# Optimization experiments

Measured on AMD Instinct MI355X. Metric: run time of the kernel, lower is better.

Reference implementation:

```python
import jax, jax.numpy as jnp
import numpy as np

THR = 10.0           # spike threshold (all layers, igarss2023 config)
LEAK1, LEAK2, LEAK3 = 9.0, 1.0, 0.0  # subtractive leak per layer
POOL1_K, POOL1_S = 7, 6
POOL2_K, POOL2_S = 2, 2
WTA_BLOCK = 2        # local spatial WTA window


def conv2d_same(x, w):
    # x: (B,C,H,W), w: (O,I,kh,kw)
    return jax.lax.conv_general_dilated(
        x, w, window_strides=(1, 1), padding='SAME',
        dimension_numbers=('NCHW', 'OIHW', 'NCHW'))


def maxpool(x, k, s):
    return jax.lax.reduce_window(
        x, -jnp.inf, jax.lax.max, (1, 1, k, k), (1, 1, s, s), 'VALID')


def wta(mem, spk, block=WTA_BLOCK):
    """Winner-take-all lateral inhibition ('both' mode):
    (1) channel competition: only the channel with max membrane at each
        spatial location may spike; (2) local spatial competition: only the
        max-membrane neuron within each block x block window of each map
        may spike. Requires H,W divisible by block."""
    C = mem.shape[1]
    ch_win = jnp.argmax(mem, axis=1)                         # (B,H,W)
    ch_mask = jax.nn.one_hot(ch_win, C, axis=1, dtype=mem.dtype)  # (B,C,H,W)
    loc = jax.lax.reduce_window(
        mem, -jnp.inf, jax.lax.max,
        (1, 1, block, block), (1, 1, block, block), 'VALID')
    loc_up = jnp.repeat(jnp.repeat(loc, block, axis=2), block, axis=3)
    sp_mask = (mem >= loc_up).astype(mem.dtype)
    return spk * ch_mask * sp_mask


def lif_step(mem, inp, leak, use_wta):
    # integrate -> threshold -> WTA -> reset-to-zero -> subtractive leak
    mem = mem + inp
    spk = (mem >= THR).astype(mem.dtype)
    if use_wta:
        spk = wta(mem, spk)
    mem = jnp.where(spk > 0, 0.0, mem)
    mem = jnp.maximum(mem - leak, 0.0)
    return mem, spk


def setup_inputs() -> dict:
    key = jax.random.key(0)
    k0, k1, k2, k3 = jax.random.split(key, 4)
    T, B, H, W = 20, 8, 256, 256
    x = jax.random.uniform(k0, (T, B, 1, H, W), dtype=jnp.float32)
    # STDP-style weights are non-negative in [0,1)
    w1 = jax.random.uniform(k1, (4, 1, 5, 5), dtype=jnp.float32)
    w2 = jax.random.uniform(k2, (36, 4, 5, 5), dtype=jnp.float32)
    w3 = jax.random.uniform(k3, (1, 36, 7, 7), dtype=jnp.float32)
    return {"x": x, "w1": w1, "w2": w2, "w3": w3}


def reference(x, w1, w2, w3):
    T, B, _, H, W = x.shape
    H1, W1 = H, W                                   # conv1 SAME
    H2 = (H1 - POOL1_K) // POOL1_S + 1              # 42
    W2 = (W1 - POOL1_K) // POOL1_S + 1
    H3 = (H2 - POOL2_K) // POOL2_S + 1              # 21
    W3 = (W2 - POOL2_K) // POOL2_S + 1
    C1, C2, C3 = w1.shape[0], w2.shape[0], w3.shape[0]

    m1_0 = jnp.zeros((B, C1, H1, W1), x.dtype)
    m2_0 = jnp.zeros((B, C2, H2, W2), x.dtype)
    m3_0 = jnp.zeros((B, C3, H3, W3), x.dtype)

    def step(carry, xt):
        m1, m2, m3 = carry
        m1, s1 = lif_step(m1, conv2d_same(xt, w1), LEAK1, True)
        p1 = maxpool(s1, POOL1_K, POOL1_S)
        m2, s2 = lif_step(m2, conv2d_same(p1, w2), LEAK2, True)
        p2 = maxpool(s2, POOL2_K, POOL2_S)
        m3, s3 = lif_step(m3, conv2d_same(p2, w3), LEAK3, False)
        return (m1, m2, m3), s3

    _, cls_spikes = jax.lax.scan(step, (m1_0, m2_0, m3_0), x)
    return cls_spikes  # (T, B, n_classes, H3, W3)
```

## Files before the change

### kernel.cpp

```cpp
#include <hip/hip_runtime.h>
#include <stdint.h>

#define THR 10.0f
#define AGT __HIP_MEMORY_SCOPE_AGENT

static constexpr size_t OFF_P2  = 1048576;
static constexpr size_t OFF_BAR = 1245184;

static __device__ __forceinline__ uint32_t ldu32(const uint32_t* p) {
    return __hip_atomic_load(p, __ATOMIC_RELAXED, AGT);
}
static __device__ __forceinline__ void stu32(uint32_t* p, uint32_t v) {
    __hip_atomic_store(p, v, __ATOMIC_RELAXED, AGT);
}
static __device__ __forceinline__ void stu16(uint16_t* p, uint16_t v) {
    __hip_atomic_store(p, v, __ATOMIC_RELAXED, AGT);
}
static __device__ __forceinline__ uint32_t rmwread(uint32_t* p) {
    return __hip_atomic_fetch_add(p, 0u, __ATOMIC_RELAXED, AGT);
}

__global__ __launch_bounds__(256) void zero_bar(uint32_t* __restrict__ bar) {
    if (threadIdx.x < 256) bar[threadIdx.x] = 0u;
}

__device__ __forceinline__ void gbar(uint32_t* bar, int bid, uint32_t n) {
    __syncthreads();
    if (threadIdx.x == 0) {
        uint32_t* base = bar + (bid >> 6) * 32;
        uint32_t a = __hip_atomic_fetch_add(base, 1u, __ATOMIC_RELAXED, AGT);
        if (a == 64u * n - 1u)
            __hip_atomic_fetch_add(base + 16, 1u, __ATOMIC_RELAXED, AGT);
        while (rmwread(base + 16) < n)
            __builtin_amdgcn_s_sleep(2);
    }
    __syncthreads();
}

__global__ __launch_bounds__(256, 2) void spike_persist(
    const float* __restrict__ x,
    const float* __restrict__ w1,
    const float* __restrict__ w2,
    const float* __restrict__ w3,
    float* __restrict__ out,
    uint8_t* __restrict__ s1b,
    uint8_t* __restrict__ p2b,
    uint32_t* __restrict__ bar)
{
    __shared__ union {
        float    xs[2112];
        uint32_t st32[527];
    } u;
    __shared__ float    ps[400];
    __shared__ float    mem_s[1296];
    __shared__ float    bm_s[324];
    __shared__ int      wc_s[36];
    __shared__ uint32_t p2a[18];

    const int tid = threadIdx.x;
    const int bid = blockIdx.x;
    uint32_t nbar = 0;

    const int b1 = bid >> 6;
    const int r0 = (bid & 63) * 4;
    const int tr = tid >> 7, tc = tid & 127;
    const int py = r0 + 2 * tr;
    const int px = 2 * tc;

    const int tIdx = bid & 63;
    const int b2 = bid >> 6;
    const int tyi = tIdx >> 3, txi = tIdx & 7;
    const int oy2 = tyi < 5 ? 6 * tyi : 30 + 4 * (tyi - 5);
    const int ox2 = txi < 5 ? 6 * txi : 30 + 4 * (txi - 5);
    const int th2 = tyi < 5 ? 6 : 4;
    const int tw2 = txi < 5 ? 6 : 4;
    const int wave = tid >> 6, lane = tid & 63;
    const int pr = lane / 6, pc = lane - 6 * pr;
    const bool act = (pr < th2) && (pc < tw2);
    const int prA = pr > 5 ? 0 : pr, pcA = pc;

    const int lid3 = (bid & 63) * 4 + wave;
    const int kyl = lane / 7, kxl = lane % 7;

    float w3v[36];
#pragma unroll
    for (int c = 0; c < 36; c++) w3v[c] = (lane < 49) ? w3[c * 49 + lane] : 0.f;

    float m1r[4][2][2];
#pragma unroll
    for (int c = 0; c < 4; c++)
#pragma unroll
        for (int dy = 0; dy < 2; dy++)
#pragma unroll
            for (int dx = 0; dx < 2; dx++) m1r[c][dy][dx] = 0.f;
    float m2r[9];
#pragma unroll
    for (int i = 0; i < 9; i++) m2r[i] = 0.f;
    float m3r[2] = {0.f, 0.f};

    for (int k = 0; k < 12; k++) {
        for (int tt = 0; tt < 2; tt++) {
            const int t = 2 * k + tt;
            if (t >= 20) break;
            uint16_t* s1w = reinterpret_cast<uint16_t*>(s1b + (size_t)(t & 3) * 262144);
            const float* xb = x + ((size_t)t * 8 + b1) * 65536;
            __syncthreads();
#pragma unroll
            for (int i = 0; i < 9; i++) {
                int idx = tid + i * 256;
                if (idx < 2112) {
                    int row = idx / 264, col = idx - row * 264;
                    int gy = r0 + row - 2, gx = col - 2;
                    float v = 0.f;
                    if (gy >= 0 && gy < 256 && gx >= 0 && gx < 256) v = xb[gy * 256 + gx];
                    u.xs[idx] = v;
                }
            }
            __syncthreads();

            float p[6][6];
#pragma unroll
            for (int i = 0; i < 6; i++)
#pragma unroll
                for (int j = 0; j < 6; j++)
                    p[i][j] = u.xs[(2 * tr + i) * 264 + 2 * tc + j];

            float acc[4][2][2];
#pragma unroll
            for (int c = 0; c < 4; c++)
#pragma unroll
                for (int dy = 0; dy < 2; dy++)
#pragma unroll
                    for (int dx = 0; dx < 2; dx++) acc[c][dy][dx] = 0.f;
#pragma unroll
            for (int c = 0; c < 4; c++)
#pragma unroll
                for (int ky = 0; ky < 5; ky++)
#pragma unroll
                    for (int kx = 0; kx < 5; kx++) {
                        float w = w1[c * 25 + ky * 5 + kx];
#pragma unroll
                        for (int dy = 0; dy < 2; dy++)
#pragma unroll
                            for (int dx = 0; dx < 2; dx++)
                                acc[c][dy][dx] = fmaf(p[dy + ky][dx + kx], w, acc[c][dy][dx]);
                    }

            float mem[4][2][2];
#pragma unroll
            for (int c = 0; c < 4; c++)
#pragma unroll
                for (int dy = 0; dy < 2; dy++)
#pragma unroll
                    for (int dx = 0; dx < 2; dx++)
                        mem[c][dy][dx] = m1r[c][dy][dx] + acc[c][dy][dx];

            int wc[2][2];
#pragma unroll
            for (int dy = 0; dy < 2; dy++)
#pragma unroll
                for (int dx = 0; dx < 2; dx++) {
                    int w = 0; float mx = mem[0][dy][dx];
#pragma unroll
                    for (int c = 1; c < 4; c++) {
                        float v = mem[c][dy][dx];
                        if (v > mx) { mx = v; w = c; }
                    }
                    wc[dy][dx] = w;
                }

            float bm[4];
#pragma unroll
            for (int c = 0; c < 4; c++)
                bm[c] = fmaxf(fmaxf(mem[c][0][0], mem[c][0][1]), fmaxf(mem[c][1][0], mem[c][1][1]));

            uint32_t bits = 0;
#pragma unroll
            for (int c = 0; c < 4; c++)
#pragma unroll
                for (int dy = 0; dy < 2; dy++)
#pragma unroll
                    for (int dx = 0; dx < 2; dx++) {
                        float m = mem[c][dy][dx];
                        bool s = (m >= THR) && (wc[dy][dx] == c) && (m >= bm[c]);
                        m1r[c][dy][dx] = fmaxf((s ? 0.f : m) - 9.0f, 0.f);
                        bits |= (s ? 1u : 0u) << (c * 4 + dy * 2 + dx);
                    }
            stu16(s1w + ((size_t)(b1 * 128 + (r0 >> 1) + tr)) * 128 + tc, (uint16_t)bits);
        }

        for (int tt = 0; tt < 2; tt++) {
            const int tl = 2 * k - 4 + tt;
            if (tl < 0 || tl >= 20) continue;
            const uint32_t* pb32 = reinterpret_cast<const uint32_t*>(
                p2b + (size_t)(tl % 6) * 32768);
#pragma unroll
            for (int rep = 0; rep < 2; rep++) {
                int o = lid3 + rep * 256;
                if (o < 441) {
                    int rr = o / 21, cl = o - rr * 21;
                    int yy = rr + kyl - 3, xx = cl + kxl - 3;
                    bool inb = (lane < 49) && yy >= 0 && yy < 21 && xx >= 0 && xx < 21;
                    uint32_t lo = 0, hi = 0;
                    if (inb) {
                        const uint32_t* pc = pb32 + (((size_t)b2 * 441 + yy * 21 + xx) << 1);
                        lo = ldu32(pc);
                        hi = ldu32(pc + 1);
                    }
                    float accv = 0.f;
#pragma unroll
                    for (int c = 0; c < 32; c++) accv += ((lo >> c) & 1u) ? w3v[c] : 0.f;
#pragma unroll
                    for (int c = 0; c < 4; c++)  accv += ((hi >> c) & 1u) ? w3v[32 + c] : 0.f;
#pragma unroll
                    for (int off = 32; off; off >>= 1) accv += __shfl_xor(accv, off, 64);
                    float memv3 = m3r[rep] + accv;
                    bool s = memv3 >= THR;
                    if (lane == 0) out[(size_t)tl * 3528 + b2 * 441 + o] = s ? 1.f : 0.f;
                    m3r[rep] = fmaxf(s ? 0.f : memv3, 0.f);
                }
            }
        }

        for (int tt = 0; tt < 2; tt++) {
            const int tb = 2 * k - 2 + tt;
            if (tb < 0 || tb >= 20) continue;
            const uint32_t* s1r32 = reinterpret_cast<const uint32_t*>(
                s1b + (size_t)(tb & 3) * 262144);
            uint32_t* p2w32 = reinterpret_cast<uint32_t*>(p2b + (size_t)(tb % 6) * 32768);

            const int rb0 = 3 * oy2 - 6;
            const int cb0 = (3 * ox2 - 6) >> 1;

            __syncthreads();
#pragma unroll
            for (int i = 0; i < 3; i++) {
                int idx = tid + i * 256;
                if (idx < 527) {
                    int row = idx / 17, w = idx - row * 17;
                    int grow = rb0 + row, gcol = cb0 + w;
                    uint32_t v = 0;
                    if (grow >= 0 && grow < 128 && gcol >= 0 && gcol < 64)
                        v = ldu32(s1r32 + ((size_t)b2 * 128 + grow) * 64 + gcol);
                    u.st32[idx] = v;
                }
            }
            __syncthreads();

            if (tid < 100) {
                int r = tid / 10, cc2 = tid - 10 * r;
                int gy = oy2 - 2 + r, gx = ox2 - 2 + cc2;
                uint32_t accb = 0;
                if (r < th2 + 4 && cc2 < tw2 + 4 && gy >= 0 && gy < 42 && gx >= 0 && gx < 42) {
                    const uint16_t* st16 = reinterpret_cast<const uint16_t*>(u.st32);
#pragma unroll
                    for (int kr = 0; kr < 4; kr++)
#pragma unroll
                        for (int kc = 0; kc < 4; kc++) {
                            uint32_t m = (kr < 3) ? (kc < 3 ? 0xFu : 0x5u)
                                                  : (kc < 3 ? 0x3u : 0x1u);
                            uint32_t v = st16[(3 * r + kr) * 34 + 3 * cc2 + kc];
                            accb |= v & (m * 0x1111u);
                        }
                }
#pragma unroll
                for (int ic = 0; ic < 4; ic++)
                    ps[ic * 100 + tid] = ((accb >> (4 * ic)) & 0xFu) ? 1.f : 0.f;
            }
            __syncthreads();

            float pv[4][5][5];
#pragma unroll
            for (int ic = 0; ic < 4; ic++)
#pragma unroll
                for (int i = 0; i < 5; i++)
#pragma unroll
                    for (int j = 0; j < 5; j++)
                        pv[ic][i][j] = ps[ic * 100 + (prA + i) * 10 + (pcA + j)];

            float memv[9];
            for (int cc = 0; cc < 9; cc++) {
                int c = cc * 4 + wave;
                const float* wr = w2 + (size_t)__builtin_amdgcn_readfirstlane(c) * 100;
                float accv = 0.f;
#pragma unroll
                for (int ic = 0; ic < 4; ic++)
#pragma unroll
                    for (int i = 0; i < 5; i++)
#pragma unroll
                        for (int j = 0; j < 5; j++)
                            accv = fmaf(pv[ic][i][j], wr[ic * 25 + i * 5 + j], accv);
                float m = act ? (m2r[cc] + accv) : -1e30f;
                memv[cc] = m;
                if (lane < 36) mem_s[c * 36 + lane] = m;
            }
            __syncthreads();

            if (tid < 36) {
                float mx = mem_s[tid]; int w = 0;
#pragma unroll
                for (int c = 1; c < 36; c++) {
                    float v = mem_s[c * 36 + tid];
                    if (v > mx) { mx = v; w = c; }
                }
                wc_s[tid] = w;
            }
#pragma unroll
            for (int i = 0; i < 2; i++) {
                int idx = tid + i * 256;
                if (idx < 324) {
                    int c = idx / 9, blk = idx - 9 * c;
                    int br = blk / 3, bc2 = blk - 3 * br;
                    int l0 = 12 * br + 2 * bc2;
                    float a = mem_s[c * 36 + l0],     bb2 = mem_s[c * 36 + l0 + 1];
                    float d = mem_s[c * 36 + l0 + 6], e   = mem_s[c * 36 + l0 + 7];
                    bm_s[idx] = fmaxf(fmaxf(a, bb2), fmaxf(d, e));
                }
            }
            if (tid < 18) p2a[tid] = 0;
            __syncthreads();

            const int blkl = (pr >> 1) * 3 + (pc >> 1);
            for (int cc = 0; cc < 9; cc++) {
                int c = cc * 4 + wave;
                if (act) {
                    float m = memv[cc];
                    bool s = (m >= THR) && (wc_s[lane] == c) && (m >= bm_s[c * 9 + blkl]);
                    m2r[cc] = fmaxf((s ? 0.f : m) - 1.0f, 0.f);
                }
            }

#pragma unroll
            for (int i = 0; i < 2; i++) {
                int idx = tid + i * 256;
                if (idx < 324) {
                    int c = idx / 9, blk = idx - 9 * c;
                    int br = blk / 3, bc2 = blk - 3 * br;
                    if (2 * br < th2 && 2 * bc2 < tw2) {
                        int l0 = 12 * br + 2 * bc2;
                        float bmv = bm_s[idx];
                        bool any = false;
#pragma unroll
                        for (int kk = 0; kk < 4; kk++) {
                            int l = l0 + (kk >> 1) * 6 + (kk & 1);
                            float m = mem_s[c * 36 + l];
                            any |= (m >= THR) && (wc_s[l] == c) && (m >= bmv);
                        }
                        if (any)
                            atomicOr(&p2a[(blk << 1) + (c >> 5)], 1u << (c & 31));
                    }
                }
            }
            __syncthreads();

            if (tid < 9) {
                int br = tid / 3, bc2 = tid - 3 * br;
                if (2 * br < th2 && 2 * bc2 < tw2) {
                    int cell = b2 * 441 + ((oy2 >> 1) + br) * 21 + (ox2 >> 1) + bc2;
                    uint32_t* dst = p2w32 + ((size_t)cell << 1);
                    stu32(dst, p2a[tid * 2]);
                    stu32(dst + 1, p2a[tid * 2 + 1]);
                }
            }
        }

        if (k < 11) gbar(bar, bid, ++nbar);
    }
}

extern "C" void kernel_launch(void* const* d_in, const int* in_sizes, int n_in,
                              void* d_out, int out_size, void* d_ws, size_t ws_size,
                              hipStream_t stream) {
    const float* x  = (const float*)d_in[0];
    const float* w1 = (const float*)d_in[1];
    const float* w2 = (const float*)d_in[2];
    const float* w3 = (const float*)d_in[3];
    float* out = (float*)d_out;
    uint8_t* s1 = (uint8_t*)d_ws;
    uint8_t* p2 = (uint8_t*)d_ws + OFF_P2;
    uint32_t* bar = (uint32_t*)((char*)d_ws + OFF_BAR);

    zero_bar<<<1, 256, 0, stream>>>(bar);

    void* args[] = {(void*)&x, (void*)&w1, (void*)&w2, (void*)&w3,
                    (void*)&out, (void*)&s1, (void*)&p2, (void*)&bar};
    hipLaunchCooperativeKernel((void*)spike_persist, dim3(512), dim3(256),
                               args, 0, stream);
}
```

Before: 459.1 us.

## Batch four timesteps per grid barrier and prefetch cross-stage inputs into registers

Each pipeline stage now processes four timesteps between grid barriers instead of two, cutting the number of grid-wide barriers from 11 to 6. The stage-1 and pooled-spike ring buffers grow from 4/6 slots to 8, and the workspace offsets are enlarged to fit. Stage-2 and stage-3 inputs for all four timesteps are loaded into registers at the start of each round, and the address and bounds math is hoisted out of the loop. The cost is deeper pipeline fill and drain, higher register pressure from the prefetch arrays, and a larger workspace.

```diff
diff --git a/kernel.cpp b/kernel.cpp
--- a/kernel.cpp
+++ b/kernel.cpp
@@ -4,8 +4,8 @@
 #define THR 10.0f
 #define AGT __HIP_MEMORY_SCOPE_AGENT
 
-static constexpr size_t OFF_P2  = 1048576;
-static constexpr size_t OFF_BAR = 1245184;
+static constexpr size_t OFF_P2  = 2097152;
+static constexpr size_t OFF_BAR = 2359296;
 
 static __device__ __forceinline__ uint32_t ldu32(const uint32_t* p) {
     return __hip_atomic_load(p, __ATOMIC_RELAXED, AGT);
@@ -64,8 +64,6 @@
     const int b1 = bid >> 6;
     const int r0 = (bid & 63) * 4;
     const int tr = tid >> 7, tc = tid & 127;
-    const int py = r0 + 2 * tr;
-    const int px = 2 * tc;
 
     const int tIdx = bid & 63;
     const int b2 = bid >> 6;
@@ -86,6 +84,40 @@
 #pragma unroll
     for (int c = 0; c < 36; c++) w3v[c] = (lane < 49) ? w3[c * 49 + lane] : 0.f;
 
+    int aoff[9]; bool aval[9];
+#pragma unroll
+    for (int i = 0; i < 9; i++) {
+        int idx = tid + i * 256;
+        int row = idx / 264, col = idx - row * 264;
+        int gy = r0 + row - 2, gx = col - 2;
+        aval[i] = (idx < 2112) && gy >= 0 && gy < 256 && gx >= 0 && gx < 256;
+        aoff[i] = gy * 256 + gx;
+    }
+    const size_t s1soff = ((size_t)(b1 * 128 + (r0 >> 1) + tr)) * 128 + tc;
+
+    const int rb0 = 3 * oy2 - 6;
+    const int cb0 = (3 * ox2 - 6) >> 1;
+    int boff[3]; bool bval[3];
+#pragma unroll
+    for (int i = 0; i < 3; i++) {
+        int idx = tid + i * 256;
+        int row = idx / 17, w = idx - row * 17;
+        int grow = rb0 + row, gcol = cb0 + w;
+        bval[i] = (idx < 527) && grow >= 0 && grow < 128 && gcol >= 0 && gcol < 64;
+        boff[i] = (b2 * 128 + grow) * 64 + gcol;
+    }
+
+    bool l3in[2], l3v[2]; int l3o[2];
+#pragma unroll
+    for (int rep = 0; rep < 2; rep++) {
+        int o = lid3 + rep * 256;
+        int rr = o / 21, cl = o - rr * 21;
+        int yy = rr + kyl - 3, xx = cl + kxl - 3;
+        l3in[rep] = o < 441;
+        l3v[rep] = (o < 441) && (lane < 49) && yy >= 0 && yy < 21 && xx >= 0 && xx < 21;
+        l3o[rep] = (b2 * 441 + yy * 21 + xx) << 1;
+    }
+
     float m1r[4][2][2];
 #pragma unroll
     for (int c = 0; c < 4; c++)
@@ -98,273 +130,282 @@
     for (int i = 0; i < 9; i++) m2r[i] = 0.f;
     float m3r[2] = {0.f, 0.f};
 
-    for (int k = 0; k < 12; k++) {
-        for (int tt = 0; tt < 2; tt++) {
-            const int t = 2 * k + tt;
-            if (t >= 20) break;
-            uint16_t* s1w = reinterpret_cast<uint16_t*>(s1b + (size_t)(t & 3) * 262144);
-            const float* xb = x + ((size_t)t * 8 + b1) * 65536;
-            __syncthreads();
-#pragma unroll
-            for (int i = 0; i < 9; i++) {
-                int idx = tid + i * 256;
-                if (idx < 2112) {
-                    int row = idx / 264, col = idx - row * 264;
-                    int gy = r0 + row - 2, gx = col - 2;
-                    float v = 0.f;
-                    if (gy >= 0 && gy < 256 && gx >= 0 && gx < 256) v = xb[gy * 256 + gx];
-                    u.xs[idx] = v;
-                }
-            }
-            __syncthreads();
-
-            float p[6][6];
-#pragma unroll
-            for (int i = 0; i < 6; i++)
-#pragma unroll
-                for (int j = 0; j < 6; j++)
-                    p[i][j] = u.xs[(2 * tr + i) * 264 + 2 * tc + j];
-
-            float acc[4][2][2];
-#pragma unroll
-            for (int c = 0; c < 4; c++)
-#pragma unroll
-                for (int dy = 0; dy < 2; dy++)
-#pragma unroll
-                    for (int dx = 0; dx < 2; dx++) acc[c][dy][dx] = 0.f;
-#pragma unroll
-            for (int c = 0; c < 4; c++)
-#pragma unroll
-                for (int ky = 0; ky < 5; ky++)
-#pragma unroll
-                    for (int kx = 0; kx < 5; kx++) {
-                        float w = w1[c * 25 + ky * 5 + kx];
-#pragma unroll
-                        for (int dy = 0; dy < 2; dy++)
-#pragma unroll
-                            for (int dx = 0; dx < 2; dx++)
-                                acc[c][dy][dx] = fmaf(p[dy + ky][dx + kx], w, acc[c][dy][dx]);
-                    }
-
-            float mem[4][2][2];
-#pragma unroll
-            for (int c = 0; c < 4; c++)
-#pragma unroll
-                for (int dy = 0; dy < 2; dy++)
-#pragma unroll
-                    for (int dx = 0; dx < 2; dx++)
-                        mem[c][dy][dx] = m1r[c][dy][dx] + acc[c][dy][dx];
-
-            int wc[2][2];
-#pragma unroll
-            for (int dy = 0; dy < 2; dy++)
-#pragma unroll
-                for (int dx = 0; dx < 2; dx++) {
-                    int w = 0; float mx = mem[0][dy][dx];
-#pragma unroll
-                    for (int c = 1; c < 4; c++) {
-                        float v = mem[c][dy][dx];
-                        if (v > mx) { mx = v; w = c; }
-                    }
-                    wc[dy][dx] = w;
-                }
-
-            float bm[4];
-#pragma unroll
-            for (int c = 0; c < 4; c++)
-                bm[c] = fmaxf(fmaxf(mem[c][0][0], mem[c][0][1]), fmaxf(mem[c][1][0], mem[c][1][1]));
-
-            uint32_t bits = 0;
-#pragma unroll
-            for (int c = 0; c < 4; c++)
-#pragma unroll
-                for (int dy = 0; dy < 2; dy++)
-#pragma unroll
-                    for (int dx = 0; dx < 2; dx++) {
-                        float m = mem[c][dy][dx];
-                        bool s = (m >= THR) && (wc[dy][dx] == c) && (m >= bm[c]);
-                        m1r[c][dy][dx] = fmaxf((s ? 0.f : m) - 9.0f, 0.f);
-                        bits |= (s ? 1u : 0u) << (c * 4 + dy * 2 + dx);
-                    }
-            stu16(s1w + ((size_t)(b1 * 128 + (r0 >> 1) + tr)) * 128 + tc, (uint16_t)bits);
-        }
-
-        for (int tt = 0; tt < 2; tt++) {
-            const int tl = 2 * k - 4 + tt;
-            if (tl < 0 || tl >= 20) continue;
-            const uint32_t* pb32 = reinterpret_cast<const uint32_t*>(
-                p2b + (size_t)(tl % 6) * 32768);
-#pragma unroll
-            for (int rep = 0; rep < 2; rep++) {
-                int o = lid3 + rep * 256;
-                if (o < 441) {
-                    int rr = o / 21, cl = o - rr * 21;
-                    int yy = rr + kyl - 3, xx = cl + kxl - 3;
-                    bool inb = (lane < 49) && yy >= 0 && yy < 21 && xx >= 0 && xx < 21;
-                    uint32_t lo = 0, hi = 0;
-                    if (inb) {
-                        const uint32_t* pc = pb32 + (((size_t)b2 * 441 + yy * 21 + xx) << 1);
-                        lo = ldu32(pc);
-                        hi = ldu32(pc + 1);
-                    }
-                    float accv = 0.f;
-#pragma unroll
-                    for (int c = 0; c < 32; c++) accv += ((lo >> c) & 1u) ? w3v[c] : 0.f;
-#pragma unroll
-                    for (int c = 0; c < 4; c++)  accv += ((hi >> c) & 1u) ? w3v[32 + c] : 0.f;
-#pragma unroll
-                    for (int off = 32; off; off >>= 1) accv += __shfl_xor(accv, off, 64);
-                    float memv3 = m3r[rep] + accv;
-                    bool s = memv3 >= THR;
-                    if (lane == 0) out[(size_t)tl * 3528 + b2 * 441 + o] = s ? 1.f : 0.f;
-                    m3r[rep] = fmaxf(s ? 0.f : memv3, 0.f);
-                }
+    for (int k = 0; k < 7; k++) {
+        uint32_t pfB[4][3];
+#pragma unroll
+        for (int tt = 0; tt < 4; tt++) {
+            int tb = 4 * k - 4 + tt;
+            if (tb >= 0 && tb < 20) {
+                const uint32_t* s1r32 = reinterpret_cast<const uint32_t*>(
+                    s1b + (size_t)(tb & 7) * 262144);
+#pragma unroll
+                for (int i = 0; i < 3; i++)
+                    pfB[tt][i] = bval[i] ? ldu32(s1r32 + boff[i]) : 0u;
             }
         }
-
-        for (int tt = 0; tt < 2; tt++) {
-            const int tb = 2 * k - 2 + tt;
-            if (tb < 0 || tb >= 20) continue;
-            const uint32_t* s1r32 = reinterpret_cast<const uint32_t*>(
-                s1b + (size_t)(tb & 3) * 262144);
-            uint32_t* p2w32 = reinterpret_cast<uint32_t*>(p2b + (size_t)(tb % 6) * 32768);
-
-            const int rb0 = 3 * oy2 - 6;
-            const int cb0 = (3 * ox2 - 6) >> 1;
-
-            __syncthreads();
-#pragma unroll
-            for (int i = 0; i < 3; i++) {
-                int idx = tid + i * 256;
-                if (idx < 527) {
-                    int row = idx / 17, w = idx - row * 17;
-                    int grow = rb0 + row, gcol = cb0 + w;
-                    uint32_t v = 0;
-                    if (grow >= 0 && grow < 128 && gcol >= 0 && gcol < 64)
-                        v = ldu32(s1r32 + ((size_t)b2 * 128 + grow) * 64 + gcol);
-                    u.st32[idx] = v;
-                }
-            }
-            __syncthreads();
-
-            if (tid < 100) {
-                int r = tid / 10, cc2 = tid - 10 * r;
-                int gy = oy2 - 2 + r, gx = ox2 - 2 + cc2;
-                uint32_t accb = 0;
-                if (r < th2 + 4 && cc2 < tw2 + 4 && gy >= 0 && gy < 42 && gx >= 0 && gx < 42) {
-                    const uint16_t* st16 = reinterpret_cast<const uint16_t*>(u.st32);
-#pragma unroll
-                    for (int kr = 0; kr < 4; kr++)
-#pragma unroll
-                        for (int kc = 0; kc < 4; kc++) {
-                            uint32_t m = (kr < 3) ? (kc < 3 ? 0xFu : 0x5u)
-                                                  : (kc < 3 ? 0x3u : 0x1u);
-                            uint32_t v = st16[(3 * r + kr) * 34 + 3 * cc2 + kc];
-                            accb |= v & (m * 0x1111u);
-                        }
-                }
-#pragma unroll
-                for (int ic = 0; ic < 4; ic++)
-                    ps[ic * 100 + tid] = ((accb >> (4 * ic)) & 0xFu) ? 1.f : 0.f;
-            }
-            __syncthreads();
-
-            float pv[4][5][5];
-#pragma unroll
-            for (int ic = 0; ic < 4; ic++)
-#pragma unroll
-                for (int i = 0; i < 5; i++)
-#pragma unroll
-                    for (int j = 0; j < 5; j++)
-                        pv[ic][i][j] = ps[ic * 100 + (prA + i) * 10 + (pcA + j)];
-
-            float memv[9];
-            for (int cc = 0; cc < 9; cc++) {
-                int c = cc * 4 + wave;
-                const float* wr = w2 + (size_t)__builtin_amdgcn_readfirstlane(c) * 100;
-                float accv = 0.f;
-#pragma unroll
-                for (int ic = 0; ic < 4; ic++)
-#pragma unroll
-                    for (int i = 0; i < 5; i++)
-#pragma unroll
-                        for (int j = 0; j < 5; j++)
-                            accv = fmaf(pv[ic][i][j], wr[ic * 25 + i * 5 + j], accv);
-                float m = act ? (m2r[cc] + accv) : -1e30f;
-                memv[cc] = m;
-                if (lane < 36) mem_s[c * 36 + lane] = m;
-            }
-            __syncthreads();
-
-            if (tid < 36) {
-                float mx = mem_s[tid]; int w = 0;
-#pragma unroll
-                for (int c = 1; c < 36; c++) {
-                    float v = mem_s[c * 36 + tid];
-                    if (v > mx) { mx = v; w = c; }
-                }
-                wc_s[tid] = w;
-            }
-#pragma unroll
-            for (int i = 0; i < 2; i++) {
-                int idx = tid + i * 256;
-                if (idx < 324) {
-                    int c = idx / 9, blk = idx - 9 * c;
-                    int br = blk / 3, bc2 = blk - 3 * br;
-                    int l0 = 12 * br + 2 * bc2;
-                    float a = mem_s[c * 36 + l0],     bb2 = mem_s[c * 36 + l0 + 1];
-                    float d = mem_s[c * 36 + l0 + 6], e   = mem_s[c * 36 + l0 + 7];
-                    bm_s[idx] = fmaxf(fmaxf(a, bb2), fmaxf(d, e));
-                }
-            }
-            if (tid < 18) p2a[tid] = 0;
-            __syncthreads();
-
-            const int blkl = (pr >> 1) * 3 + (pc >> 1);
-            for (int cc = 0; cc < 9; cc++) {
-                int c = cc * 4 + wave;
-                if (act) {
-                    float m = memv[cc];
-                    bool s = (m >= THR) && (wc_s[lane] == c) && (m >= bm_s[c * 9 + blkl]);
-                    m2r[cc] = fmaxf((s ? 0.f : m) - 1.0f, 0.f);
-                }
-            }
-
-#pragma unroll
-            for (int i = 0; i < 2; i++) {
-                int idx = tid + i * 256;
-                if (idx < 324) {
-                    int c = idx / 9, blk = idx - 9 * c;
-                    int br = blk / 3, bc2 = blk - 3 * br;
-                    if (2 * br < th2 && 2 * bc2 < tw2) {
-                        int l0 = 12 * br + 2 * bc2;
-                        float bmv = bm_s[idx];
-                        bool any = false;
-#pragma unroll
-                        for (int kk = 0; kk < 4; kk++) {
-                            int l = l0 + (kk >> 1) * 6 + (kk & 1);
-                            float m = mem_s[c * 36 + l];
-                            any |= (m >= THR) && (wc_s[l] == c) && (m >= bmv);
-                        }
-                        if (any)
-                            atomicOr(&p2a[(blk << 1) + (c >> 5)], 1u << (c & 31));
-                    }
-                }
-            }
-            __syncthreads();
-
-            if (tid < 9) {
-                int br = tid / 3, bc2 = tid - 3 * br;
-                if (2 * br < th2 && 2 * bc2 < tw2) {
-                    int cell = b2 * 441 + ((oy2 >> 1) + br) * 21 + (ox2 >> 1) + bc2;
-                    uint32_t* dst = p2w32 + ((size_t)cell << 1);
-                    stu32(dst, p2a[tid * 2]);
-                    stu32(dst + 1, p2a[tid * 2 + 1]);
+        uint32_t pfLlo[4][2], pfLhi[4][2];
+#pragma unroll
+        for (int tt = 0; tt < 4; tt++) {
+            int tl = 4 * k - 8 + tt;
+            if (tl >= 0 && tl < 20) {
+                const uint32_t* pb32 = reinterpret_cast<const uint32_t*>(
+                    p2b + (size_t)(tl & 7) * 32768);
+#pragma unroll
+                for (int rep = 0; rep < 2; rep++) {
+                    pfLlo[tt][rep] = l3v[rep] ? ldu32(pb32 + l3o[rep]) : 0u;
+                    pfLhi[tt][rep] = l3v[rep] ? ldu32(pb32 + l3o[rep] + 1) : 0u;
                 }
             }
         }
 
-        if (k < 11) gbar(bar, bid, ++nbar);
+#pragma unroll
+        for (int tt = 0; tt < 4; tt++) {
+            const int t = 4 * k + tt;
+            if (t < 20) {
+                uint16_t* s1w = reinterpret_cast<uint16_t*>(s1b + (size_t)(t & 7) * 262144);
+                const float* xb = x + ((size_t)t * 8 + b1) * 65536;
+                __syncthreads();
+#pragma unroll
+                for (int i = 0; i < 9; i++) {
+                    int idx = tid + i * 256;
+                    if (idx < 2112) u.xs[idx] = aval[i] ? xb[aoff[i]] : 0.f;
+                }
+                __syncthreads();
+
+                const float2* xs2 = reinterpret_cast<const float2*>(u.xs);
+                float p[6][6];
+#pragma unroll
+                for (int i = 0; i < 6; i++)
+#pragma unroll
+                    for (int j = 0; j < 3; j++) {
+                        float2 v = xs2[(2 * tr + i) * 132 + tc + j];
+                        p[i][2 * j] = v.x; p[i][2 * j + 1] = v.y;
+                    }
+
+                float acc[4][2][2];
+#pragma unroll
+                for (int c = 0; c < 4; c++)
+#pragma unroll
+                    for (int dy = 0; dy < 2; dy++)
+#pragma unroll
+                        for (int dx = 0; dx < 2; dx++) acc[c][dy][dx] = 0.f;
+#pragma unroll
+                for (int c = 0; c < 4; c++)
+#pragma unroll
+                    for (int ky = 0; ky < 5; ky++)
+#pragma unroll
+                        for (int kx = 0; kx < 5; kx++) {
+                            float w = w1[c * 25 + ky * 5 + kx];
+#pragma unroll
+                            for (int dy = 0; dy < 2; dy++)
+#pragma unroll
+                                for (int dx = 0; dx < 2; dx++)
+                                    acc[c][dy][dx] = fmaf(p[dy + ky][dx + kx], w, acc[c][dy][dx]);
+                        }
+
+                float mem[4][2][2];
+#pragma unroll
+                for (int c = 0; c < 4; c++)
+#pragma unroll
+                    for (int dy = 0; dy < 2; dy++)
+#pragma unroll
+                        for (int dx = 0; dx < 2; dx++)
+                            mem[c][dy][dx] = m1r[c][dy][dx] + acc[c][dy][dx];
+
+                int wc[2][2];
+#pragma unroll
+                for (int dy = 0; dy < 2; dy++)
+#pragma unroll
+                    for (int dx = 0; dx < 2; dx++) {
+                        int w = 0; float mx = mem[0][dy][dx];
+#pragma unroll
+                        for (int c = 1; c < 4; c++) {
+                            float v = mem[c][dy][dx];
+                            if (v > mx) { mx = v; w = c; }
+                        }
+                        wc[dy][dx] = w;
+                    }
+
+                float bm[4];
+#pragma unroll
+                for (int c = 0; c < 4; c++)
+                    bm[c] = fmaxf(fmaxf(mem[c][0][0], mem[c][0][1]),
+                                  fmaxf(mem[c][1][0], mem[c][1][1]));
+
+                uint32_t bits = 0;
+#pragma unroll
+                for (int c = 0; c < 4; c++)
+#pragma unroll
+                    for (int dy = 0; dy < 2; dy++)
+#pragma unroll
+                        for (int dx = 0; dx < 2; dx++) {
+                            float m = mem[c][dy][dx];
+                            bool s = (m >= THR) && (wc[dy][dx] == c) && (m >= bm[c]);
+                            m1r[c][dy][dx] = fmaxf((s ? 0.f : m) - 9.0f, 0.f);
+                            bits |= (s ? 1u : 0u) << (c * 4 + dy * 2 + dx);
+                        }
+                stu16(reinterpret_cast<uint16_t*>(s1w) + s1soff, (uint16_t)bits);
+            }
+        }
+
+#pragma unroll
+        for (int tt = 0; tt < 4; tt++) {
+            const int tl = 4 * k - 8 + tt;
+            if (tl >= 0 && tl < 20) {
+#pragma unroll
+                for (int rep = 0; rep < 2; rep++) {
+                    if (l3in[rep]) {
+                        int o = lid3 + rep * 256;
+                        uint32_t lo = pfLlo[tt][rep], hi = pfLhi[tt][rep];
+                        float accv = 0.f;
+#pragma unroll
+                        for (int c = 0; c < 32; c++) accv += ((lo >> c) & 1u) ? w3v[c] : 0.f;
+#pragma unroll
+                        for (int c = 0; c < 4; c++)  accv += ((hi >> c) & 1u) ? w3v[32 + c] : 0.f;
+#pragma unroll
+                        for (int off = 32; off; off >>= 1) accv += __shfl_xor(accv, off, 64);
+                        float memv3 = m3r[rep] + accv;
+                        bool s = memv3 >= THR;
+                        if (lane == 0) out[(size_t)tl * 3528 + b2 * 441 + o] = s ? 1.f : 0.f;
+                        m3r[rep] = fmaxf(s ? 0.f : memv3, 0.f);
+                    }
+                }
+            }
+        }
+
+#pragma unroll
+        for (int tt = 0; tt < 4; tt++) {
+            const int tb = 4 * k - 4 + tt;
+            if (tb >= 0 && tb < 20) {
+                uint32_t* p2w32 = reinterpret_cast<uint32_t*>(p2b + (size_t)(tb & 7) * 32768);
+
+                __syncthreads();
+#pragma unroll
+                for (int i = 0; i < 3; i++) {
+                    int idx = tid + i * 256;
+                    if (idx < 527) u.st32[idx] = pfB[tt][i];
+                }
+                __syncthreads();
+
+                if (tid < 100) {
+                    int r = tid / 10, cc2 = tid - 10 * r;
+                    int gy = oy2 - 2 + r, gx = ox2 - 2 + cc2;
+                    uint32_t accb = 0;
+                    if (r < th2 + 4 && cc2 < tw2 + 4 && gy >= 0 && gy < 42 && gx >= 0 && gx < 42) {
+                        const uint16_t* st16 = reinterpret_cast<const uint16_t*>(u.st32);
+#pragma unroll
+                        for (int kr = 0; kr < 4; kr++)
+#pragma unroll
+                            for (int kc = 0; kc < 4; kc++) {
+                                uint32_t m = (kr < 3) ? (kc < 3 ? 0xFu : 0x5u)
+                                                      : (kc < 3 ? 0x3u : 0x1u);
+                                uint32_t v = st16[(3 * r + kr) * 34 + 3 * cc2 + kc];
+                                accb |= v & (m * 0x1111u);
+                            }
+                    }
+#pragma unroll
+                    for (int ic = 0; ic < 4; ic++)
+                        ps[ic * 100 + tid] = ((accb >> (4 * ic)) & 0xFu) ? 1.f : 0.f;
+                }
+                __syncthreads();
+
+                float pv[4][5][5];
+#pragma unroll
+                for (int ic = 0; ic < 4; ic++)
+#pragma unroll
+                    for (int i = 0; i < 5; i++)
+#pragma unroll
+                        for (int j = 0; j < 5; j++)
+                            pv[ic][i][j] = ps[ic * 100 + (prA + i) * 10 + (pcA + j)];
+
+                float memv[9];
+                for (int cc = 0; cc < 9; cc++) {
+                    int c = cc * 4 + wave;
+                    const float* wr = w2 + (size_t)__builtin_amdgcn_readfirstlane(c) * 100;
+                    float accv = 0.f;
+#pragma unroll
+                    for (int ic = 0; ic < 4; ic++)
+#pragma unroll
+                        for (int i = 0; i < 5; i++)
+#pragma unroll
+                            for (int j = 0; j < 5; j++)
+                                accv = fmaf(pv[ic][i][j], wr[ic * 25 + i * 5 + j], accv);
+                    float m = act ? (m2r[cc] + accv) : -1e30f;
+                    memv[cc] = m;
+                    if (lane < 36) mem_s[c * 36 + lane] = m;
+                }
+                __syncthreads();
+
+                if (tid < 36) {
+                    float mx = mem_s[tid]; int w = 0;
+#pragma unroll
+                    for (int c = 1; c < 36; c++) {
+                        float v = mem_s[c * 36 + tid];
+                        if (v > mx) { mx = v; w = c; }
+                    }
+                    wc_s[tid] = w;
+                }
+#pragma unroll
+                for (int i = 0; i < 2; i++) {
+                    int idx = tid + i * 256;
+                    if (idx < 324) {
+                        int c = idx / 9, blk = idx - 9 * c;
+                        int br = blk / 3, bc2 = blk - 3 * br;
+                        int l0 = 12 * br + 2 * bc2;
+                        float a = mem_s[c * 36 + l0],     bb2 = mem_s[c * 36 + l0 + 1];
+                        float d = mem_s[c * 36 + l0 + 6], e   = mem_s[c * 36 + l0 + 7];
+                        bm_s[idx] = fmaxf(fmaxf(a, bb2), fmaxf(d, e));
+                    }
+                }
+                if (tid < 18) p2a[tid] = 0;
+                __syncthreads();
+
+                const int blkl = (pr >> 1) * 3 + (pc >> 1);
+                for (int cc = 0; cc < 9; cc++) {
+                    int c = cc * 4 + wave;
+                    if (act) {
+                        float m = memv[cc];
+                        bool s = (m >= THR) && (wc_s[lane] == c) && (m >= bm_s[c * 9 + blkl]);
+                        m2r[cc] = fmaxf((s ? 0.f : m) - 1.0f, 0.f);
+                    }
+                }
+
+#pragma unroll
+                for (int i = 0; i < 2; i++) {
+                    int idx = tid + i * 256;
+                    if (idx < 324) {
+                        int c = idx / 9, blk = idx - 9 * c;
+                        int br = blk / 3, bc2 = blk - 3 * br;
+                        if (2 * br < th2 && 2 * bc2 < tw2) {
+                            int l0 = 12 * br + 2 * bc2;
+                            float bmv = bm_s[idx];
+                            bool any = false;
+#pragma unroll
+                            for (int kk = 0; kk < 4; kk++) {
+                                int l = l0 + (kk >> 1) * 6 + (kk & 1);
+                                float m = mem_s[c * 36 + l];
+                                any |= (m >= THR) && (wc_s[l] == c) && (m >= bmv);
+                            }
+                            if (any)
+                                atomicOr(&p2a[(blk << 1) + (c >> 5)], 1u << (c & 31));
+                        }
+                    }
+                }
+                __syncthreads();
+
+                if (tid < 9) {
+                    int br = tid / 3, bc2 = tid - 3 * br;
+                    if (2 * br < th2 && 2 * bc2 < tw2) {
+                        int cell = b2 * 441 + ((oy2 >> 1) + br) * 21 + (ox2 >> 1) + bc2;
+                        uint32_t* dst = p2w32 + ((size_t)cell << 1);
+                        stu32(dst, p2a[tid * 2]);
+                        stu32(dst + 1, p2a[tid * 2 + 1]);
+                    }
+                }
+            }
+        }
+
+        if (k < 6) gbar(bar, bid, ++nbar);
     }
 }
 
```

Measured after the change: 453.5 us. Within noise of the previous version (-1.2%).
